# Optimization experiments

Hardware: AMD Instinct MI355X
Metric: run time of the kernel (lower is better)

The kernel has to match this reference:

```python
import jax, jax.numpy as jnp
import numpy as np

EMBED_DIM = 1024
NUM_HEADS = 16
HEAD_DIM = EMBED_DIM // NUM_HEADS
R_QKV = 256
R_OUT = 256
B, T = 4, 2048


def setup_inputs() -> dict:
    key = jax.random.key(0)
    k1, k2, k3, k4, k5 = jax.random.split(key, 5)
    s = 0.02
    return {
        "x": jax.random.normal(k1, (B, T, EMBED_DIM), dtype=jnp.float32),
        "W_qkv_v": jax.random.normal(k2, (R_QKV, EMBED_DIM), dtype=jnp.float32) * s,
        "W_qkv_u": jax.random.normal(k3, (3 * EMBED_DIM, R_QKV), dtype=jnp.float32) * s,
        "W_o_v": jax.random.normal(k4, (R_OUT, EMBED_DIM), dtype=jnp.float32) * s,
        "W_o_u": jax.random.normal(k5, (EMBED_DIM, R_OUT), dtype=jnp.float32) * s,
    }


def reference(x, W_qkv_v, W_qkv_u, W_o_v, W_o_u):
    Bq, Tq, C = x.shape
    H, D = NUM_HEADS, HEAD_DIM
    # low-rank qkv projection: x @ V^T @ U^T (torch Linear weight is [out,in])
    qkv = (x @ W_qkv_v.T) @ W_qkv_u.T  # [B,T,3C]
    q, k, v = jnp.split(qkv, 3, axis=-1)
    # split heads -> [B,H,T,D]
    q = q.reshape(Bq, Tq, H, D).transpose(0, 2, 1, 3)
    k = k.reshape(Bq, Tq, H, D).transpose(0, 2, 1, 3)
    v = v.reshape(Bq, Tq, H, D).transpose(0, 2, 1, 3)
    scale = 1.0 / jnp.sqrt(jnp.asarray(D, dtype=x.dtype))
    scores = jnp.einsum('bhtd,bhsd->bhts', q, k) * scale  # [B,H,T,T]
    # softmax in fp32 then cast back, matching torch.softmax(dtype=float32)
    attn = jax.nn.softmax(scores.astype(jnp.float32), axis=-1).astype(q.dtype)
    y = jnp.einsum('bhts,bhsd->bhtd', attn, v)  # [B,H,T,D]
    y = y.transpose(0, 2, 1, 3).reshape(Bq, Tq, C)  # merge heads
    # low-rank output projection
    y = (y @ W_o_v.T) @ W_o_u.T
    return y
```

## Files before the change

### kernel.cpp

```cpp
#include <hip/hip_runtime.h>
#include <hip/hip_bf16.h>

typedef __attribute__((ext_vector_type(8))) short short8;
typedef __attribute__((ext_vector_type(4))) float f32x4;
typedef __attribute__((ext_vector_type(16))) float f32x16;
typedef unsigned short u16;
typedef unsigned int u32;

__device__ __forceinline__ void gload_lds16(const void* g, void* l) {
  typedef const __attribute__((address_space(1))) u32 gu32;
  typedef __attribute__((address_space(3))) u32 lu32;
  __builtin_amdgcn_global_load_lds((gu32*)g, (lu32*)l, 16, 0, 0);
}

__device__ __forceinline__ u16 f2bf(float f) {
  union { float f; u32 u; } v; v.f = f;
  u32 u = v.u + 0x7FFFu + ((v.u >> 16) & 1u);
  return (u16)(u >> 16);
}

__device__ __forceinline__ u32 cvtpk(float lo, float hiv) {
  u32 r;
  asm("v_cvt_pk_bf16_f32 %0, %1, %2" : "=v"(r) : "v"(lo), "v"(hiv));
  return r;
}

__device__ __forceinline__ void plswap(u32& a, u32& b) {
  asm("v_permlane32_swap_b32 %0, %1" : "+v"(a), "+v"(b));
}

__device__ __forceinline__ float fexp2(float x) {
  float r;
  asm("v_exp_f32 %0, %1" : "=v"(r) : "v"(x));
  return r;
}

__device__ __forceinline__ short8 lds_read8(const u16* base, int byteoff) {
  return *(const short8*)((const char*)base + byteoff);
}

__global__ __launch_bounds__(256) void cast_w_kernel(
    const float* __restrict__ wv, const float* __restrict__ wu,
    const float* __restrict__ wov, const float* __restrict__ wou,
    u16* __restrict__ dst) {
  const long N0 = 262144, N1 = N0 + 786432, N2 = N1 + 262144, N3 = N2 + 262144;
  long i = (long)(blockIdx.x * 256 + threadIdx.x) * 8;
  if (i >= N3) return;
  const float* s;
  if (i < N0) s = wv + i;
  else if (i < N1) s = wu + (i - N0);
  else if (i < N2) s = wov + (i - N1);
  else s = wou + (i - N2);
  float4 a = *(const float4*)s;
  float4 b = *(const float4*)(s + 4);
  short8 o;
  o[0] = (short)f2bf(a.x); o[1] = (short)f2bf(a.y);
  o[2] = (short)f2bf(a.z); o[3] = (short)f2bf(a.w);
  o[4] = (short)f2bf(b.x); o[5] = (short)f2bf(b.y);
  o[6] = (short)f2bf(b.z); o[7] = (short)f2bf(b.w);
  *(short8*)(dst + i) = o;
}

template<int BM, int BN, int MR, int NR, typename OutT>
__global__ __launch_bounds__(256) void gemm_bt(
    OutT* __restrict__ C, const u16* __restrict__ A, const u16* __restrict__ B,
    int N, int K) {
  __shared__ u16 As[BM * 64];
  __shared__ u16 Bs[BN * 64];
  const int tid = threadIdx.x;
  const int l = tid & 63, w = tid >> 6;
  const int wr = w >> 1, wc = w & 1;
  const int bm = blockIdx.x * BM, bn = blockIdx.y * BN;
  const int srow = l >> 3, sslot = (l & 7) ^ srow;

  f32x4 acc[MR][NR] = {};

  const u16* Ag = A + (long)(bm + srow) * K + sslot * 8;
  const u16* Bg = B + (long)(bn + srow) * K + sslot * 8;
  constexpr int CA = BM / 32, CB = BN / 32;

  for (int kt = 0; kt < K; kt += 64) {
#pragma unroll
    for (int c = 0; c < CA; ++c) {
      int ch = w * CA + c;
      gload_lds16(Ag + (long)ch * 8 * K + kt, (char*)As + ch * 1024);
    }
#pragma unroll
    for (int c = 0; c < CB; ++c) {
      int ch = w * CB + c;
      gload_lds16(Bg + (long)ch * 8 * K + kt, (char*)Bs + ch * 1024);
    }
    __syncthreads();
    short8 af[MR][2], bf[NR][2];
#pragma unroll
    for (int i = 0; i < MR; ++i)
#pragma unroll
      for (int kk = 0; kk < 2; ++kk) {
        int row = wr * (MR * 16) + i * 16 + (l & 15);
        af[i][kk] = lds_read8(As, row * 128 + (((kk * 4 + (l >> 4)) ^ (l & 7)) * 16));
      }
#pragma unroll
    for (int j = 0; j < NR; ++j)
#pragma unroll
      for (int kk = 0; kk < 2; ++kk) {
        int col = wc * (NR * 16) + j * 16 + (l & 15);
        bf[j][kk] = lds_read8(Bs, col * 128 + (((kk * 4 + (l >> 4)) ^ (l & 7)) * 16));
      }
#pragma unroll
    for (int kk = 0; kk < 2; ++kk)
#pragma unroll
      for (int i = 0; i < MR; ++i)
#pragma unroll
        for (int j = 0; j < NR; ++j)
          acc[i][j] = __builtin_amdgcn_mfma_f32_16x16x32_bf16(
              af[i][kk], bf[j][kk], acc[i][j], 0, 0, 0);
    __syncthreads();
  }
#pragma unroll
  for (int i = 0; i < MR; ++i)
#pragma unroll
    for (int j = 0; j < NR; ++j) {
      int row = bm + wr * (MR * 16) + i * 16 + (l >> 4) * 4;
      int col = bn + wc * (NR * 16) + j * 16 + (l & 15);
#pragma unroll
      for (int r = 0; r < 4; ++r) {
        if constexpr (sizeof(OutT) == 4) {
          C[(long)(row + r) * N + col] = acc[i][j][r];
        } else {
          ((u16*)C)[(long)(row + r) * N + col] = f2bf(acc[i][j][r]);
        }
      }
    }
}

__global__ __launch_bounds__(256) void gemm_a32(
    u16* __restrict__ C, const float* __restrict__ A, const u16* __restrict__ B,
    int N, int K) {
  constexpr int BM = 64, BN = 64, MR = 2, NR = 2;
  __shared__ u16 As[BM * 64];
  __shared__ u16 Bs[BN * 64];
  const int tid = threadIdx.x;
  const int l = tid & 63, w = tid >> 6;
  const int wr = w >> 1, wc = w & 1;
  const int bm = blockIdx.x * BM, bn = blockIdx.y * BN;
  const int srow = l >> 3, sslot = (l & 7) ^ srow;

  f32x4 acc[MR][NR] = {};
  const u16* Bg = B + (long)(bn + srow) * K + sslot * 8;

  for (int kt = 0; kt < K; kt += 64) {
#pragma unroll
    for (int c = 0; c < 2; ++c) {
      int ch = w * 2 + c;
      gload_lds16(Bg + (long)ch * 8 * K + kt, (char*)Bs + ch * 1024);
    }
#pragma unroll
    for (int it = 0; it < 2; ++it) {
      int c = tid + it * 256;
      int row = c >> 3, slot = c & 7;
      const float* src = A + (long)(bm + row) * K + kt + slot * 8;
      float4 a = *(const float4*)src;
      float4 b = *(const float4*)(src + 4);
      union { u32 u[4]; short8 s; } pk;
      pk.u[0] = cvtpk(a.x, a.y);
      pk.u[1] = cvtpk(a.z, a.w);
      pk.u[2] = cvtpk(b.x, b.y);
      pk.u[3] = cvtpk(b.z, b.w);
      *(short8*)((char*)As + row * 128 + ((slot ^ (row & 7)) * 16)) = pk.s;
    }
    __syncthreads();
    short8 af[MR][2], bf[NR][2];
#pragma unroll
    for (int i = 0; i < MR; ++i)
#pragma unroll
      for (int kk = 0; kk < 2; ++kk) {
        int row = wr * (MR * 16) + i * 16 + (l & 15);
        af[i][kk] = lds_read8(As, row * 128 + (((kk * 4 + (l >> 4)) ^ (l & 7)) * 16));
      }
#pragma unroll
    for (int j = 0; j < NR; ++j)
#pragma unroll
      for (int kk = 0; kk < 2; ++kk) {
        int col = wc * (NR * 16) + j * 16 + (l & 15);
        bf[j][kk] = lds_read8(Bs, col * 128 + (((kk * 4 + (l >> 4)) ^ (l & 7)) * 16));
      }
#pragma unroll
    for (int kk = 0; kk < 2; ++kk)
#pragma unroll
      for (int i = 0; i < MR; ++i)
#pragma unroll
        for (int j = 0; j < NR; ++j)
          acc[i][j] = __builtin_amdgcn_mfma_f32_16x16x32_bf16(
              af[i][kk], bf[j][kk], acc[i][j], 0, 0, 0);
    __syncthreads();
  }
#pragma unroll
  for (int i = 0; i < MR; ++i)
#pragma unroll
    for (int j = 0; j < NR; ++j) {
      int row = bm + wr * (MR * 16) + i * 16 + (l >> 4) * 4;
      int col = bn + wc * (NR * 16) + j * 16 + (l & 15);
#pragma unroll
      for (int r = 0; r < 4; ++r)
        C[(long)(row + r) * N + col] = f2bf(acc[i][j][r]);
    }
}

__global__ __launch_bounds__(256) void vtrans_kernel(
    u16* __restrict__ Vt, const u16* __restrict__ QKV) {
  constexpr int T = 2048, LDQ = 3072;
  __shared__ u16 L[64 * 80];
  const int tid = threadIdx.x;
  const int t0 = blockIdx.x * 64, bh = blockIdx.y;
  const int b = bh >> 4, h = bh & 15;
  const u16* src = QKV + (long)b * T * LDQ + 2048 + h * 64;
#pragma unroll
  for (int it = 0; it < 2; ++it) {
    int row = (tid >> 3) + it * 32;
    int d0 = (tid & 7) * 8;
    short8 v = *(const short8*)(src + (long)(t0 + row) * LDQ + d0);
#pragma unroll
    for (int j = 0; j < 8; ++j)
      L[(d0 + j) * 80 + row] = (u16)(short)v[j];
  }
  __syncthreads();
  u16* dst = Vt + (long)bh * 64 * T + t0;
#pragma unroll
  for (int it = 0; it < 2; ++it) {
    int d = (tid >> 3) + it * 32;
    int c = (tid & 7) * 8;
    *(short8*)(dst + (long)d * T + c) = *(const short8*)(&L[d * 80 + c]);
  }
}

__global__ __launch_bounds__(512, 4) void attn_kernel(
    u16* __restrict__ Y, const u16* __restrict__ QKV, const u16* __restrict__ Vt) {
  constexpr int T = 2048, LDQ = 3072, NT = T / 64;
  constexpr float SC = 0.18033688011112042f;
  __shared__ u16 SMEM[24576];
  const int tid = threadIdx.x, l = tid & 63, w = tid >> 6;
  const int lq = l & 31, hi = l >> 5;
  const int qt = blockIdx.x, bh = blockIdx.y;
  const int b = bh >> 4, h = bh & 15;
  const long base = (long)b * T * LDQ;
  const int q0 = qt * 256 + w * 32;

  short8 qf[4];
#pragma unroll
  for (int ks = 0; ks < 4; ++ks)
    qf[ks] = *(const short8*)(QKV + base + (long)(q0 + lq) * LDQ + h * 64 +
                              ks * 16 + hi * 8);

  const short8 ONES = {(short)0x3F80, (short)0x3F80, (short)0x3F80, (short)0x3F80,
                       (short)0x3F80, (short)0x3F80, (short)0x3F80, (short)0x3F80};

  f32x16 o0 = {}, o1 = {}, olr = {};

  const int c = tid;
  const int kr = c >> 3, ds = (c & 7) ^ (kr & 7);
  const u16* Kg = QKV + base + 1024 + h * 64;
  const u16* Vg = Vt + (long)bh * 64 * T;

  auto STAGE = [&](int kt, int s) {
    u16* Kd = SMEM + s * 8192;
    u16* Vd = Kd + 4096;
    gload_lds16(Kg + (long)(kt + kr) * LDQ + ds * 8, (char*)Kd + c * 16);
    gload_lds16(Vg + (long)kr * T + kt + ds * 8, (char*)Vd + c * 16);
  };

  const int pslA[4] = {((0 + hi) ^ (lq & 7)) * 16, ((2 + hi) ^ (lq & 7)) * 16,
                       ((4 + hi) ^ (lq & 7)) * 16, ((6 + hi) ^ (lq & 7)) * 16};

  auto COMPUTE = [&](const u16* Ks, const u16* Vs) {
    f32x16 p0 = {}, p1 = {};
    __builtin_amdgcn_s_setprio(1);
#pragma unroll
    for (int ks = 0; ks < 4; ++ks) {
      short8 ka = lds_read8(Ks, lq * 128 + pslA[ks]);
      short8 kb = lds_read8(Ks, (32 + lq) * 128 + pslA[ks]);
      p0 = __builtin_amdgcn_mfma_f32_32x32x16_bf16(ka, qf[ks], p0, 0, 0, 0);
      p1 = __builtin_amdgcn_mfma_f32_32x32x16_bf16(kb, qf[ks], p1, 0, 0, 0);
    }
    __builtin_amdgcn_s_setprio(0);
    p0 = p0 * SC;
    p1 = p1 * SC;
#pragma unroll
    for (int r = 0; r < 16; ++r) p0[r] = fexp2(p0[r]);
#pragma unroll
    for (int r = 0; r < 16; ++r) p1[r] = fexp2(p1[r]);
    __builtin_amdgcn_s_setprio(1);
#pragma unroll
    for (int ks = 0; ks < 4; ++ks) {
      const f32x16& ps = (ks < 2) ? p0 : p1;
      const int r0 = (ks & 1) * 8;
      u32 uA = cvtpk(ps[r0 + 0], ps[r0 + 1]);
      u32 uB = cvtpk(ps[r0 + 2], ps[r0 + 3]);
      u32 uC = cvtpk(ps[r0 + 4], ps[r0 + 5]);
      u32 uD = cvtpk(ps[r0 + 6], ps[r0 + 7]);
      plswap(uA, uC);
      plswap(uB, uD);
      union { u32 u[4]; short8 s; } pb;
      pb.u[0] = uA; pb.u[1] = uB; pb.u[2] = uC; pb.u[3] = uD;
      short8 va = lds_read8(Vs, lq * 128 + pslA[ks]);
      short8 vb = lds_read8(Vs, (32 + lq) * 128 + pslA[ks]);
      o0 = __builtin_amdgcn_mfma_f32_32x32x16_bf16(va, pb.s, o0, 0, 0, 0);
      o1 = __builtin_amdgcn_mfma_f32_32x32x16_bf16(vb, pb.s, o1, 0, 0, 0);
      olr = __builtin_amdgcn_mfma_f32_32x32x16_bf16(ONES, pb.s, olr, 0, 0, 0);
    }
    __builtin_amdgcn_s_setprio(0);
  };

  STAGE(0, 0);
  STAGE(64, 1);
  for (int t = 0; t < NT; ++t) {
    if (t + 1 < NT) {
      asm volatile("s_waitcnt vmcnt(2)" ::: "memory");
    } else {
      asm volatile("s_waitcnt vmcnt(0)" ::: "memory");
    }
    __builtin_amdgcn_s_barrier();
    __builtin_amdgcn_sched_barrier(0);
    if (t + 2 < NT) STAGE((t + 2) * 64, (t + 2) % 3);
    const u16* Ks = SMEM + (t % 3) * 8192;
    COMPUTE(Ks, Ks + 4096);
  }

  __syncthreads();
  float inv = 1.0f / olr[0];
  const int row = w * 32 + lq;
#pragma unroll
  for (int df = 0; df < 2; ++df)
#pragma unroll
    for (int r = 0; r < 16; ++r) {
      int d = df * 32 + (r & 3) + 8 * (r >> 2) + 4 * hi;
      float v = (df ? o1[r] : o0[r]) * inv;
      *(u16*)((char*)SMEM + row * 128 + (((d >> 3) ^ (row & 7)) * 16) + (d & 7) * 2) =
          f2bf(v);
    }
  __syncthreads();
#pragma unroll
  for (int it = 0; it < 4; ++it) {
    int cc = tid + it * 512;
    int q = cc >> 3, g = cc & 7;
    int pg = g ^ (q & 7);
    short8 vv = *(const short8*)((const char*)SMEM + q * 128 + pg * 16);
    *(short8*)(Y + (long)(b * T + qt * 256 + q) * 1024 + h * 64 + g * 8) = vv;
  }
}

__global__ void ws_too_small_kernel(float* out) { out[0] = 3.0e38f; }

extern "C" void kernel_launch(void* const* d_in, const int* in_sizes, int n_in,
                              void* d_out, int out_size, void* d_ws, size_t ws_size,
                              hipStream_t stream) {
  (void)in_sizes; (void)n_in; (void)out_size;
  const float* x   = (const float*)d_in[0];
  const float* wv  = (const float*)d_in[1];
  const float* wu  = (const float*)d_in[2];
  const float* wov = (const float*)d_in[3];
  const float* wou = (const float*)d_in[4];
  float* out = (float*)d_out;
  u16* ws = (u16*)d_ws;

  u16* wvb  = ws;
  u16* wub  = ws + 262144;
  u16* wovb = ws + 1048576;
  u16* woub = ws + 1310720;
  u16* t    = ws + 1572864;
  u16* qkv  = ws + 3670016;
  u16* vt   = ws + 28835840;
  u16* yb   = ws + 37224448;
  u16* z    = ws + 45613056;

  if (ws_size < 95420416ull) {
    ws_too_small_kernel<<<1, 1, 0, stream>>>(out);
    return;
  }

  cast_w_kernel<<<dim3(768), dim3(256), 0, stream>>>(wv, wu, wov, wou, ws);
  gemm_a32<<<dim3(128, 4), dim3(256), 0, stream>>>(t, x, wvb, 256, 1024);
  gemm_bt<128, 128, 4, 4, u16><<<dim3(64, 24), dim3(256), 0, stream>>>(qkv, t, wub, 3072, 256);
  vtrans_kernel<<<dim3(32, 64), dim3(256), 0, stream>>>(vt, qkv);
  attn_kernel<<<dim3(8, 64), dim3(512), 0, stream>>>(yb, qkv, vt);
  gemm_bt<64, 64, 2, 2, u16><<<dim3(128, 4), dim3(256), 0, stream>>>(z, yb, wovb, 256, 1024);
  gemm_bt<128, 128, 4, 4, float><<<dim3(64, 8), dim3(256), 0, stream>>>(out, z, woub, 1024, 256);
}
```

Baseline: 174.9 us.

## Give each attention wave two query sub-tiles to reuse K/V LDS fragments

The attention kernel now runs 256 threads (4 waves) per block, and each wave handles 64 query rows as two 32-row sub-tiles instead of 32 rows. Every K and V fragment read from LDS is reused across both sub-tiles, halving LDS reads per MFMA. Each thread issues twice as many staging loads, so the wait counts change to match, and the grid is reordered so blockIdx.x walks batch-head pairs. The cost is many more accumulator registers per wave and half as many waves per block, which may lower occupancy and the ability to hide latency.

```diff
diff --git a/kernel.cpp b/kernel.cpp
--- a/kernel.cpp
+++ b/kernel.cpp
@@ -233,79 +233,102 @@
   }
 }
 
-__global__ __launch_bounds__(512, 4) void attn_kernel(
+__global__ __launch_bounds__(256) void attn_kernel(
     u16* __restrict__ Y, const u16* __restrict__ QKV, const u16* __restrict__ Vt) {
   constexpr int T = 2048, LDQ = 3072, NT = T / 64;
   constexpr float SC = 0.18033688011112042f;
   __shared__ u16 SMEM[24576];
   const int tid = threadIdx.x, l = tid & 63, w = tid >> 6;
   const int lq = l & 31, hi = l >> 5;
-  const int qt = blockIdx.x, bh = blockIdx.y;
+  const int bh = blockIdx.x, qt = blockIdx.y;
   const int b = bh >> 4, h = bh & 15;
   const long base = (long)b * T * LDQ;
-  const int q0 = qt * 256 + w * 32;
-
-  short8 qf[4];
-#pragma unroll
-  for (int ks = 0; ks < 4; ++ks)
-    qf[ks] = *(const short8*)(QKV + base + (long)(q0 + lq) * LDQ + h * 64 +
-                              ks * 16 + hi * 8);
+  const int q0 = qt * 256 + w * 64;
+
+  short8 qfA[4], qfB[4];
+#pragma unroll
+  for (int ks = 0; ks < 4; ++ks) {
+    const u16* qp = QKV + base + h * 64 + ks * 16 + hi * 8;
+    qfA[ks] = *(const short8*)(qp + (long)(q0 + lq) * LDQ);
+    qfB[ks] = *(const short8*)(qp + (long)(q0 + 32 + lq) * LDQ);
+  }
+  asm volatile("s_waitcnt vmcnt(0)" ::: "memory");
 
   const short8 ONES = {(short)0x3F80, (short)0x3F80, (short)0x3F80, (short)0x3F80,
                        (short)0x3F80, (short)0x3F80, (short)0x3F80, (short)0x3F80};
 
-  f32x16 o0 = {}, o1 = {}, olr = {};
-
-  const int c = tid;
-  const int kr = c >> 3, ds = (c & 7) ^ (kr & 7);
+  f32x16 oA0 = {}, oA1 = {}, oB0 = {}, oB1 = {}, olrA = {}, olrB = {};
+
+  const int c0 = tid, c1 = tid + 256;
+  const int kr0 = c0 >> 3, ds0 = (c0 & 7) ^ (kr0 & 7);
+  const int kr1 = c1 >> 3, ds1 = (c1 & 7) ^ (kr1 & 7);
   const u16* Kg = QKV + base + 1024 + h * 64;
   const u16* Vg = Vt + (long)bh * 64 * T;
 
   auto STAGE = [&](int kt, int s) {
     u16* Kd = SMEM + s * 8192;
     u16* Vd = Kd + 4096;
-    gload_lds16(Kg + (long)(kt + kr) * LDQ + ds * 8, (char*)Kd + c * 16);
-    gload_lds16(Vg + (long)kr * T + kt + ds * 8, (char*)Vd + c * 16);
+    gload_lds16(Kg + (long)(kt + kr0) * LDQ + ds0 * 8, (char*)Kd + c0 * 16);
+    gload_lds16(Kg + (long)(kt + kr1) * LDQ + ds1 * 8, (char*)Kd + c1 * 16);
+    gload_lds16(Vg + (long)kr0 * T + kt + ds0 * 8, (char*)Vd + c0 * 16);
+    gload_lds16(Vg + (long)kr1 * T + kt + ds1 * 8, (char*)Vd + c1 * 16);
   };
 
   const int pslA[4] = {((0 + hi) ^ (lq & 7)) * 16, ((2 + hi) ^ (lq & 7)) * 16,
                        ((4 + hi) ^ (lq & 7)) * 16, ((6 + hi) ^ (lq & 7)) * 16};
 
   auto COMPUTE = [&](const u16* Ks, const u16* Vs) {
-    f32x16 p0 = {}, p1 = {};
+    f32x16 pA0 = {}, pA1 = {}, pB0 = {}, pB1 = {};
     __builtin_amdgcn_s_setprio(1);
 #pragma unroll
     for (int ks = 0; ks < 4; ++ks) {
       short8 ka = lds_read8(Ks, lq * 128 + pslA[ks]);
       short8 kb = lds_read8(Ks, (32 + lq) * 128 + pslA[ks]);
-      p0 = __builtin_amdgcn_mfma_f32_32x32x16_bf16(ka, qf[ks], p0, 0, 0, 0);
-      p1 = __builtin_amdgcn_mfma_f32_32x32x16_bf16(kb, qf[ks], p1, 0, 0, 0);
+      pA0 = __builtin_amdgcn_mfma_f32_32x32x16_bf16(ka, qfA[ks], pA0, 0, 0, 0);
+      pA1 = __builtin_amdgcn_mfma_f32_32x32x16_bf16(kb, qfA[ks], pA1, 0, 0, 0);
+      pB0 = __builtin_amdgcn_mfma_f32_32x32x16_bf16(ka, qfB[ks], pB0, 0, 0, 0);
+      pB1 = __builtin_amdgcn_mfma_f32_32x32x16_bf16(kb, qfB[ks], pB1, 0, 0, 0);
     }
     __builtin_amdgcn_s_setprio(0);
-    p0 = p0 * SC;
-    p1 = p1 * SC;
-#pragma unroll
-    for (int r = 0; r < 16; ++r) p0[r] = fexp2(p0[r]);
-#pragma unroll
-    for (int r = 0; r < 16; ++r) p1[r] = fexp2(p1[r]);
+    pA0 = pA0 * SC; pA1 = pA1 * SC; pB0 = pB0 * SC; pB1 = pB1 * SC;
+#pragma unroll
+    for (int r = 0; r < 16; ++r) pA0[r] = fexp2(pA0[r]);
+#pragma unroll
+    for (int r = 0; r < 16; ++r) pA1[r] = fexp2(pA1[r]);
+#pragma unroll
+    for (int r = 0; r < 16; ++r) pB0[r] = fexp2(pB0[r]);
+#pragma unroll
+    for (int r = 0; r < 16; ++r) pB1[r] = fexp2(pB1[r]);
     __builtin_amdgcn_s_setprio(1);
 #pragma unroll
     for (int ks = 0; ks < 4; ++ks) {
-      const f32x16& ps = (ks < 2) ? p0 : p1;
+      const f32x16& psA = (ks < 2) ? pA0 : pA1;
+      const f32x16& psB = (ks < 2) ? pB0 : pB1;
       const int r0 = (ks & 1) * 8;
-      u32 uA = cvtpk(ps[r0 + 0], ps[r0 + 1]);
-      u32 uB = cvtpk(ps[r0 + 2], ps[r0 + 3]);
-      u32 uC = cvtpk(ps[r0 + 4], ps[r0 + 5]);
-      u32 uD = cvtpk(ps[r0 + 6], ps[r0 + 7]);
-      plswap(uA, uC);
-      plswap(uB, uD);
-      union { u32 u[4]; short8 s; } pb;
-      pb.u[0] = uA; pb.u[1] = uB; pb.u[2] = uC; pb.u[3] = uD;
+      u32 aA = cvtpk(psA[r0 + 0], psA[r0 + 1]);
+      u32 bA = cvtpk(psA[r0 + 2], psA[r0 + 3]);
+      u32 cA = cvtpk(psA[r0 + 4], psA[r0 + 5]);
+      u32 dA = cvtpk(psA[r0 + 6], psA[r0 + 7]);
+      plswap(aA, cA);
+      plswap(bA, dA);
+      union { u32 u[4]; short8 s; } pbA;
+      pbA.u[0] = aA; pbA.u[1] = bA; pbA.u[2] = cA; pbA.u[3] = dA;
+      u32 aB = cvtpk(psB[r0 + 0], psB[r0 + 1]);
+      u32 bB = cvtpk(psB[r0 + 2], psB[r0 + 3]);
+      u32 cB = cvtpk(psB[r0 + 4], psB[r0 + 5]);
+      u32 dB = cvtpk(psB[r0 + 6], psB[r0 + 7]);
+      plswap(aB, cB);
+      plswap(bB, dB);
+      union { u32 u[4]; short8 s; } pbB;
+      pbB.u[0] = aB; pbB.u[1] = bB; pbB.u[2] = cB; pbB.u[3] = dB;
       short8 va = lds_read8(Vs, lq * 128 + pslA[ks]);
       short8 vb = lds_read8(Vs, (32 + lq) * 128 + pslA[ks]);
-      o0 = __builtin_amdgcn_mfma_f32_32x32x16_bf16(va, pb.s, o0, 0, 0, 0);
-      o1 = __builtin_amdgcn_mfma_f32_32x32x16_bf16(vb, pb.s, o1, 0, 0, 0);
-      olr = __builtin_amdgcn_mfma_f32_32x32x16_bf16(ONES, pb.s, olr, 0, 0, 0);
+      oA0 = __builtin_amdgcn_mfma_f32_32x32x16_bf16(va, pbA.s, oA0, 0, 0, 0);
+      oA1 = __builtin_amdgcn_mfma_f32_32x32x16_bf16(vb, pbA.s, oA1, 0, 0, 0);
+      olrA = __builtin_amdgcn_mfma_f32_32x32x16_bf16(ONES, pbA.s, olrA, 0, 0, 0);
+      oB0 = __builtin_amdgcn_mfma_f32_32x32x16_bf16(va, pbB.s, oB0, 0, 0, 0);
+      oB1 = __builtin_amdgcn_mfma_f32_32x32x16_bf16(vb, pbB.s, oB1, 0, 0, 0);
+      olrB = __builtin_amdgcn_mfma_f32_32x32x16_bf16(ONES, pbB.s, olrB, 0, 0, 0);
     }
     __builtin_amdgcn_s_setprio(0);
   };
@@ -314,7 +337,7 @@
   STAGE(64, 1);
   for (int t = 0; t < NT; ++t) {
     if (t + 1 < NT) {
-      asm volatile("s_waitcnt vmcnt(2)" ::: "memory");
+      asm volatile("s_waitcnt vmcnt(4)" ::: "memory");
     } else {
       asm volatile("s_waitcnt vmcnt(0)" ::: "memory");
     }
@@ -326,21 +349,24 @@
   }
 
   __syncthreads();
-  float inv = 1.0f / olr[0];
-  const int row = w * 32 + lq;
+  float invA = 1.0f / olrA[0];
+  float invB = 1.0f / olrB[0];
+  const int rowA = w * 64 + lq, rowB = rowA + 32;
 #pragma unroll
   for (int df = 0; df < 2; ++df)
 #pragma unroll
     for (int r = 0; r < 16; ++r) {
       int d = df * 32 + (r & 3) + 8 * (r >> 2) + 4 * hi;
-      float v = (df ? o1[r] : o0[r]) * inv;
-      *(u16*)((char*)SMEM + row * 128 + (((d >> 3) ^ (row & 7)) * 16) + (d & 7) * 2) =
-          f2bf(v);
+      int slot = ((d >> 3) ^ (rowA & 7)) * 16 + (d & 7) * 2;
+      float vA = (df ? oA1[r] : oA0[r]) * invA;
+      float vB = (df ? oB1[r] : oB0[r]) * invB;
+      *(u16*)((char*)SMEM + rowA * 128 + slot) = f2bf(vA);
+      *(u16*)((char*)SMEM + rowB * 128 + slot) = f2bf(vB);
     }
   __syncthreads();
 #pragma unroll
-  for (int it = 0; it < 4; ++it) {
-    int cc = tid + it * 512;
+  for (int it = 0; it < 8; ++it) {
+    int cc = tid + it * 256;
     int q = cc >> 3, g = cc & 7;
     int pg = g ^ (q & 7);
     short8 vv = *(const short8*)((const char*)SMEM + q * 128 + pg * 16);
@@ -381,7 +407,7 @@
   gemm_a32<<<dim3(128, 4), dim3(256), 0, stream>>>(t, x, wvb, 256, 1024);
   gemm_bt<128, 128, 4, 4, u16><<<dim3(64, 24), dim3(256), 0, stream>>>(qkv, t, wub, 3072, 256);
   vtrans_kernel<<<dim3(32, 64), dim3(256), 0, stream>>>(vt, qkv);
-  attn_kernel<<<dim3(8, 64), dim3(512), 0, stream>>>(yb, qkv, vt);
+  attn_kernel<<<dim3(64, 8), dim3(256), 0, stream>>>(yb, qkv, vt);
   gemm_bt<64, 64, 2, 2, u16><<<dim3(128, 4), dim3(256), 0, stream>>>(z, yb, wovb, 256, 1024);
   gemm_bt<128, 128, 4, 4, float><<<dim3(64, 8), dim3(256), 0, stream>>>(out, z, woub, 1024, 256);
 }
```

New measurement: 179.6 us. 2.7% more time.
